# Kernel tuning notes

Measured on AMD Instinct MI355X. Metric: run time of the kernel, lower is better.

## Reference

```python
import jax, jax.numpy as jnp
import numpy as np

H = 1024        # hidden_size
F = 4096        # intermediate_size
E = 8           # num_local_experts
TOP_K = 2       # num_experts_per_tok
B, S = 1, 2048


def setup_inputs() -> dict:
    key = jax.random.key(0)
    k0, k1, k2, k3 = jax.random.split(key, 4)
    hidden_states = jax.random.normal(k0, (B, S, H), dtype=jnp.float32)
    # torch nn.Linear weights: gate [E_out, in]; experts stacked on leading axis
    gate_w = jax.random.normal(k1, (E, H), dtype=jnp.float32) * 0.02
    gate_up_w = jax.random.normal(k2, (E, 2 * F, H), dtype=jnp.float32) * 0.02
    down_w = jax.random.normal(k3, (E, H, F), dtype=jnp.float32) * 0.02
    return {"hidden_states": hidden_states, "gate_w": gate_w,
            "gate_up_w": gate_up_w, "down_w": down_w}


def reference(hidden_states, gate_w, gate_up_w, down_w):
    b, s, h = hidden_states.shape
    x = hidden_states.reshape(-1, h)                      # [T, H]
    # router: softmax in float32, top-k, renormalize
    router_logits = x @ gate_w.T                          # [T, E]
    probs = jax.nn.softmax(router_logits.astype(jnp.float32), axis=-1)
    topw, sel = jax.lax.top_k(probs, TOP_K)               # [T, K]
    topw = topw / jnp.sum(topw, axis=-1, keepdims=True)
    topw = topw.astype(x.dtype)
    # combine weights [T, E]: zero for unselected experts -> same math as
    # the per-expert gather/scatter loop (full capacity, no dropped tokens)
    combine = jnp.sum(jax.nn.one_hot(sel, E, dtype=x.dtype) * topw[..., None], axis=1)
    # all experts on all tokens (dense-equivalent of masked dispatch)
    gu = jnp.einsum('th,efh->etf', x, gate_up_w)          # [E, T, 2F]
    gate, up = gu[..., :F], gu[..., F:]
    hact = up * jax.nn.gelu(gate, approximate=False)      # [E, T, F]
    expert_out = jnp.einsum('etf,ehf->eth', hact, down_w) # [E, T, H]
    out = jnp.einsum('eth,te->th', expert_out, combine)   # [T, H]
    return out.reshape(b, s, h)
```

## Files before the change

kernel.cpp:

```cpp
#include <hip/hip_runtime.h>

#define Hdim 1024
#define Fdim 4096
#define NE   8
#define NT   2048
#define MT_MAX 16
#define KSPLIT 2

typedef __attribute__((ext_vector_type(8))) short short8;
typedef __attribute__((ext_vector_type(4))) short short4v;
typedef __attribute__((ext_vector_type(4))) float f32x4;

__device__ __forceinline__ unsigned short bf16r(float f) {
  union { float fv; unsigned u; } v; v.fv = f;
  unsigned u = v.u;
  return (unsigned short)((u + 0x7FFFu + ((u >> 16) & 1u)) >> 16);
}

__global__ void k_router(const float* __restrict__ x, const float* __restrict__ gw,
                         int* __restrict__ counts, int* __restrict__ sel,
                         float* __restrict__ selw) {
  int wave = threadIdx.x >> 6;
  int l    = threadIdx.x & 63;
  int t    = blockIdx.x * 4 + wave;
  const float* xp = x + (size_t)t * Hdim;
  float acc[NE];
#pragma unroll
  for (int e = 0; e < NE; e++) acc[e] = 0.f;
  for (int h = l; h < Hdim; h += 64) {
    float xv = xp[h];
#pragma unroll
    for (int e = 0; e < NE; e++) acc[e] += xv * gw[e * Hdim + h];
  }
#pragma unroll
  for (int e = 0; e < NE; e++) {
    float v = acc[e];
#pragma unroll
    for (int off = 32; off > 0; off >>= 1) v += __shfl_down(v, off, 64);
    acc[e] = v;
  }
  if (l == 0) {
    int b0 = 0; float v0 = acc[0];
    for (int e = 1; e < NE; e++) if (acc[e] > v0) { v0 = acc[e]; b0 = e; }
    int b1 = -1; float v1 = -1e30f;
    for (int e = 0; e < NE; e++) if (e != b0 && acc[e] > v1) { v1 = acc[e]; b1 = e; }
    float w0 = 1.f / (1.f + expf(v1 - v0));
    atomicAdd(&counts[b0], 1);
    atomicAdd(&counts[b1], 1);
    sel[2 * t]     = b0;
    sel[2 * t + 1] = b1;
    selw[2 * t]     = w0;
    selw[2 * t + 1] = 1.f - w0;
  }
}

__global__ void k_scatter(const int* __restrict__ counts, const int* __restrict__ sel,
                          const float* __restrict__ selw, int* __restrict__ offsets,
                          int* __restrict__ rowids, float* __restrict__ pairw,
                          int* __restrict__ tok2slot) {
  __shared__ int soff[NE];
  __shared__ int scur[NE];
  if (threadIdx.x == 0) {
    int s = 0;
    for (int e = 0; e < NE; e++) { soff[e] = s; offsets[e] = s; s += counts[e]; scur[e] = 0; }
  }
  __syncthreads();
  for (int t = threadIdx.x; t < NT; t += blockDim.x) {
#pragma unroll
    for (int j = 0; j < 2; j++) {
      int e = sel[2 * t + j];
      int p = atomicAdd(&scur[e], 1);
      int slot = soff[e] + p;
      rowids[slot]        = t;
      pairw[slot]         = selw[2 * t + j];
      tok2slot[2 * t + j] = slot;
    }
  }
}

__global__ __launch_bounds__(256, 2)
void k_gate_up(const float* __restrict__ x, const float* __restrict__ gup,
               const int* __restrict__ counts, const int* __restrict__ offsets,
               const int* __restrict__ rowids, unsigned short* __restrict__ hact) {
  int e  = blockIdx.y >> 4;
  int mt = blockIdx.y & 15;
  int n  = counts[e];
  if (mt * 128 >= n) return;
  int base = offsets[e];
  int row0 = mt * 128;
  int f0   = blockIdx.x * 64;

  __shared__ __align__(16) unsigned short As[128][40];
  __shared__ __align__(16) unsigned short Bs[128][40];
  __shared__ int rid[128];

  int tid = threadIdx.x;
  if (tid < 128) {
    int r = row0 + tid;
    rid[tid] = (r < n) ? rowids[base + r] : rowids[base];
  }
  __syncthreads();

  int kc   = (tid & 7) * 4;
  int trow = tid >> 3;
  const float* ap[4];
  const float* bp[4];
#pragma unroll
  for (int p = 0; p < 4; p++) {
    int ar = p * 32 + trow;
    ap[p] = x + (size_t)rid[ar] * Hdim + kc;
    int f = (ar < 64) ? (f0 + ar) : (Fdim + f0 + (ar - 64));
    bp[p] = gup + ((size_t)e * 2 * Fdim + f) * Hdim + kc;
  }

  int wave = tid >> 6, lane = tid & 63;
  int wy = wave >> 1, wx = wave & 1;
  int lrow = lane & 15, lk = (lane >> 4) * 8;
  f32x4 acc[4][4] = {};

  float4 ra[4], rb[4];
#pragma unroll
  for (int p = 0; p < 4; p++) { ra[p] = *(const float4*)(ap[p]); rb[p] = *(const float4*)(bp[p]); }

  for (int k0 = 0; k0 < Hdim; k0 += 32) {
    __syncthreads();
#pragma unroll
    for (int p = 0; p < 4; p++) {
      int ar = p * 32 + trow;
      short4v sa;
      sa.x = (short)bf16r(ra[p].x); sa.y = (short)bf16r(ra[p].y);
      sa.z = (short)bf16r(ra[p].z); sa.w = (short)bf16r(ra[p].w);
      *(short4v*)&As[ar][kc] = sa;
      short4v sb;
      sb.x = (short)bf16r(rb[p].x); sb.y = (short)bf16r(rb[p].y);
      sb.z = (short)bf16r(rb[p].z); sb.w = (short)bf16r(rb[p].w);
      *(short4v*)&Bs[ar][kc] = sb;
    }
    if (k0 + 32 < Hdim) {
#pragma unroll
      for (int p = 0; p < 4; p++) {
        ra[p] = *(const float4*)(ap[p] + k0 + 32);
        rb[p] = *(const float4*)(bp[p] + k0 + 32);
      }
    }
    __syncthreads();
    short8 a[4], b[4];
#pragma unroll
    for (int i = 0; i < 4; i++) a[i] = *(const short8*)&As[wy * 64 + i * 16 + lrow][lk];
    b[0] = *(const short8*)&Bs[wx * 32 + lrow][lk];
    b[1] = *(const short8*)&Bs[wx * 32 + 16 + lrow][lk];
    b[2] = *(const short8*)&Bs[64 + wx * 32 + lrow][lk];
    b[3] = *(const short8*)&Bs[64 + wx * 32 + 16 + lrow][lk];
#pragma unroll
    for (int i = 0; i < 4; i++)
#pragma unroll
      for (int j = 0; j < 4; j++)
        acc[i][j] = __builtin_amdgcn_mfma_f32_16x16x32_bf16(a[i], b[j], acc[i][j], 0, 0, 0);
  }

  int quad = lane >> 4;
#pragma unroll
  for (int i = 0; i < 4; i++) {
#pragma unroll
    for (int r = 0; r < 4; r++) {
      int rl = row0 + wy * 64 + i * 16 + quad * 4 + r;
      if (rl < n) {
        size_t rowoff = (size_t)(base + rl) * Fdim + f0 + wx * 32;
#pragma unroll
        for (int j = 0; j < 2; j++) {
          float g = acc[i][j][r];
          float u = acc[i][j + 2][r];
          float ge = 0.5f * g * (1.f + erff(g * 0.70710678118654752f));
          hact[rowoff + j * 16 + lrow] = bf16r(u * ge);
        }
      }
    }
  }
}

__global__ __launch_bounds__(256, 2)
void k_down(const unsigned short* __restrict__ hact, const float* __restrict__ dw,
            const int* __restrict__ counts, const int* __restrict__ offsets,
            const int* __restrict__ rowids, const float* __restrict__ pairw,
            float* __restrict__ part) {
  int e  = blockIdx.y >> 4;
  int mt = blockIdx.y & 15;
  int n  = counts[e];
  if (mt * 128 >= n) return;
  int base = offsets[e];
  int row0 = mt * 128;
  int h0   = blockIdx.x * 128;
  const int KC = Fdim / KSPLIT;
  int kbeg = blockIdx.z * KC;
  int kend = kbeg + KC;

  __shared__ __align__(16) unsigned short As[128][72];
  __shared__ __align__(16) unsigned short Bs[128][72];

  int tid = threadIdx.x;
  int wave = tid >> 6, lane = tid & 63;
  int wy = wave >> 1, wx = wave & 1;
  int lrow = lane & 15, lkq = (lane >> 4) * 8;

  const unsigned short* asrc[4];
#pragma unroll
  for (int p = 0; p < 4; p++) {
    int idx = p * 256 + tid;
    int row = idx >> 3, seg = idx & 7;
    int slot = base + row0 + row;
    if (slot > NT * 2 - 1) slot = NT * 2 - 1;
    asrc[p] = hact + (size_t)slot * Fdim + seg * 8;
  }
  const float* bsrc[8];
#pragma unroll
  for (int p = 0; p < 8; p++) {
    int idx = p * 256 + tid;
    int row = idx >> 4, seg = idx & 15;
    bsrc[p] = dw + ((size_t)e * Hdim + h0 + row) * Fdim + seg * 4;
  }

  int4   raw[4];
  float4 rbw[8];
#pragma unroll
  for (int p = 0; p < 4; p++) raw[p] = *(const int4*)(asrc[p] + kbeg);
#pragma unroll
  for (int p = 0; p < 8; p++) rbw[p] = *(const float4*)(bsrc[p] + kbeg);

  f32x4 acc[4][4] = {};
  for (int k0 = kbeg; k0 < kend; k0 += 64) {
    __syncthreads();
#pragma unroll
    for (int p = 0; p < 4; p++) {
      int idx = p * 256 + tid;
      int row = idx >> 3, seg = idx & 7;
      *(int4*)&As[row][seg * 8] = raw[p];
    }
#pragma unroll
    for (int p = 0; p < 8; p++) {
      int idx = p * 256 + tid;
      int row = idx >> 4, seg = idx & 15;
      short4v sb;
      sb.x = (short)bf16r(rbw[p].x); sb.y = (short)bf16r(rbw[p].y);
      sb.z = (short)bf16r(rbw[p].z); sb.w = (short)bf16r(rbw[p].w);
      *(short4v*)&Bs[row][seg * 4] = sb;
    }
    if (k0 + 64 < kend) {
#pragma unroll
      for (int p = 0; p < 4; p++) raw[p] = *(const int4*)(asrc[p] + k0 + 64);
#pragma unroll
      for (int p = 0; p < 8; p++) rbw[p] = *(const float4*)(bsrc[p] + k0 + 64);
    }
    __syncthreads();
#pragma unroll
    for (int ks = 0; ks < 2; ks++) {
      short8 a[4], b[4];
#pragma unroll
      for (int i = 0; i < 4; i++) a[i] = *(const short8*)&As[wy * 64 + i * 16 + lrow][ks * 32 + lkq];
#pragma unroll
      for (int j = 0; j < 4; j++) b[j] = *(const short8*)&Bs[wx * 64 + j * 16 + lrow][ks * 32 + lkq];
#pragma unroll
      for (int i = 0; i < 4; i++)
#pragma unroll
        for (int j = 0; j < 4; j++)
          acc[i][j] = __builtin_amdgcn_mfma_f32_16x16x32_bf16(a[i], b[j], acc[i][j], 0, 0, 0);
    }
  }

  int quad = lane >> 4;
#pragma unroll
  for (int i = 0; i < 4; i++) {
#pragma unroll
    for (int r = 0; r < 4; r++) {
      int rl = row0 + wy * 64 + i * 16 + quad * 4 + r;
      if (rl < n) {
        int slot = base + rl;
        float wv = pairw[slot];
        float* op = part + ((size_t)blockIdx.z * (NT * 2) + slot) * Hdim + h0 + wx * 64;
#pragma unroll
        for (int j = 0; j < 4; j++)
          op[j * 16 + lrow] = wv * acc[i][j][r];
      }
    }
  }
}

__global__ __launch_bounds__(256)
void k_combine(const float* __restrict__ part, const int* __restrict__ tok2slot,
               float* __restrict__ out) {
  int idx = blockIdx.x * 256 + threadIdx.x;
  int t  = idx >> 8;
  int hc = (idx & 255) << 2;
  int s0 = tok2slot[2 * t];
  int s1 = tok2slot[2 * t + 1];
  float4 a = *(const float4*)&part[(size_t)s0 * Hdim + hc];
  float4 b = *(const float4*)&part[((size_t)(NT * 2) + s0) * Hdim + hc];
  float4 c = *(const float4*)&part[(size_t)s1 * Hdim + hc];
  float4 d = *(const float4*)&part[((size_t)(NT * 2) + s1) * Hdim + hc];
  float4 s;
  s.x = (a.x + b.x) + (c.x + d.x);
  s.y = (a.y + b.y) + (c.y + d.y);
  s.z = (a.z + b.z) + (c.z + d.z);
  s.w = (a.w + b.w) + (c.w + d.w);
  *(float4*)&out[(size_t)t * Hdim + hc] = s;
}

extern "C" void kernel_launch(void* const* d_in, const int* in_sizes, int n_in,
                              void* d_out, int out_size, void* d_ws, size_t ws_size,
                              hipStream_t stream) {
  const float* x   = (const float*)d_in[0];
  const float* gw  = (const float*)d_in[1];
  const float* gup = (const float*)d_in[2];
  const float* dwn = (const float*)d_in[3];
  float* out = (float*)d_out;

  char* ws = (char*)d_ws;
  int*   counts   = (int*)(ws + 0);
  int*   offsets  = (int*)(ws + 128);
  int*   sel      = (int*)(ws + 4096);
  float* selw     = (float*)(ws + 4096 + 16384);
  int*   rowids   = (int*)(ws + 4096 + 32768);
  float* pairw    = (float*)(ws + 4096 + 49152);
  int*   tok2slot = (int*)(ws + 4096 + 65536);
  unsigned short* hact = (unsigned short*)(ws + (1 << 20));
  float* part = (float*)(ws + (1 << 20) + ((size_t)32 << 20));

  hipMemsetAsync(ws, 0, 4096, stream);

  k_router<<<NT / 4, 256, 0, stream>>>(x, gw, counts, sel, selw);
  k_scatter<<<1, 1024, 0, stream>>>(counts, sel, selw, offsets, rowids, pairw, tok2slot);
  k_gate_up<<<dim3(Fdim / 64, NE * MT_MAX), 256, 0, stream>>>(x, gup, counts, offsets, rowids, hact);
  k_down<<<dim3(Hdim / 128, NE * MT_MAX, KSPLIT), 256, 0, stream>>>(hact, dwn, counts, offsets, rowids, pairw, part);
  k_combine<<<NT * Hdim / 4 / 256, 256, 0, stream>>>(part, tok2slot, out);
}
```

Measured before the change: 761.4 us.

## Pre-convert activations and weights to bf16 and load tiles via global_load_lds

Adds a conversion kernel that casts x, gate_up and down weights to bf16 in workspace before each GEMM. The GEMMs then stream bf16 tiles directly into LDS with global_load_lds, using an XOR swizzle instead of padding to avoid bank conflicts, and drop the per-tile in-register conversion. Inside the GEMMs this halves the bytes read per weight tile and removes the conversion ALU work. In exchange there are extra full passes that read the fp32 weights and write bf16 copies on every call, the load loop is no longer register-prefetched, and the fast path runs only when the workspace is large enough.

```diff
diff --git a/kernel.cpp b/kernel.cpp
--- a/kernel.cpp
+++ b/kernel.cpp
@@ -15,6 +15,24 @@
   union { float fv; unsigned u; } v; v.fv = f;
   unsigned u = v.u;
   return (unsigned short)((u + 0x7FFFu + ((u >> 16) & 1u)) >> 16);
+}
+
+__device__ __forceinline__ void gl_lds16(const void* g, void* l) {
+  __builtin_amdgcn_global_load_lds(
+      (const __attribute__((address_space(1))) unsigned int*)g,
+      (__attribute__((address_space(3))) unsigned int*)l, 16, 0, 0);
+}
+
+__global__ __launch_bounds__(256)
+void k_cvt(const float* __restrict__ src, unsigned short* __restrict__ dst, int n4) {
+  int stride = gridDim.x * 256;
+  for (int i = blockIdx.x * 256 + threadIdx.x; i < n4; i += stride) {
+    float4 v = *(const float4*)(src + (size_t)i * 4);
+    short4v s;
+    s.x = (short)bf16r(v.x); s.y = (short)bf16r(v.y);
+    s.z = (short)bf16r(v.z); s.w = (short)bf16r(v.w);
+    *(short4v*)(dst + (size_t)i * 4) = s;
+  }
 }
 
 __global__ void k_router(const float* __restrict__ x, const float* __restrict__ gw,
@@ -79,9 +97,9 @@
 }
 
 __global__ __launch_bounds__(256, 2)
-void k_gate_up(const float* __restrict__ x, const float* __restrict__ gup,
-               const int* __restrict__ counts, const int* __restrict__ offsets,
-               const int* __restrict__ rowids, unsigned short* __restrict__ hact) {
+void k_gate_up_bf(const unsigned short* __restrict__ xbf, const unsigned short* __restrict__ wbf,
+                  const int* __restrict__ counts, const int* __restrict__ offsets,
+                  const int* __restrict__ rowids, unsigned short* __restrict__ hact) {
   int e  = blockIdx.y >> 4;
   int mt = blockIdx.y & 15;
   int n  = counts[e];
@@ -90,8 +108,8 @@
   int row0 = mt * 128;
   int f0   = blockIdx.x * 64;
 
-  __shared__ __align__(16) unsigned short As[128][40];
-  __shared__ __align__(16) unsigned short Bs[128][40];
+  __shared__ __align__(16) unsigned short As[128][64];
+  __shared__ __align__(16) unsigned short Bs[128][64];
   __shared__ int rid[128];
 
   int tid = threadIdx.x;
@@ -101,61 +119,54 @@
   }
   __syncthreads();
 
-  int kc   = (tid & 7) * 4;
-  int trow = tid >> 3;
-  const float* ap[4];
-  const float* bp[4];
+  int crow  = tid >> 3;
+  int cphys = tid & 7;
+  const unsigned short* sa[4];
+  const unsigned short* sb[4];
 #pragma unroll
   for (int p = 0; p < 4; p++) {
-    int ar = p * 32 + trow;
-    ap[p] = x + (size_t)rid[ar] * Hdim + kc;
-    int f = (ar < 64) ? (f0 + ar) : (Fdim + f0 + (ar - 64));
-    bp[p] = gup + ((size_t)e * 2 * Fdim + f) * Hdim + kc;
-  }
-
-  int wave = tid >> 6, lane = tid & 63;
-  int wy = wave >> 1, wx = wave & 1;
-  int lrow = lane & 15, lk = (lane >> 4) * 8;
+    int R = p * 32 + crow;
+    int csrc = cphys ^ (R & 7);
+    sa[p] = xbf + (size_t)rid[R] * Hdim + csrc * 8;
+    int fr = (R < 64) ? (f0 + R) : (Fdim + f0 + (R - 64));
+    sb[p] = wbf + ((size_t)e * 2 * Fdim + fr) * Hdim + csrc * 8;
+  }
+  int w = tid >> 6, lane = tid & 63;
+  unsigned short* da[4];
+  unsigned short* db[4];
+#pragma unroll
+  for (int p = 0; p < 4; p++) {
+    da[p] = &As[0][0] + p * 2048 + w * 512;
+    db[p] = &Bs[0][0] + p * 2048 + w * 512;
+  }
+
+  int wy = w >> 1, wx = w & 1;
+  int lrow = lane & 15, cq = lane >> 4;
   f32x4 acc[4][4] = {};
 
-  float4 ra[4], rb[4];
-#pragma unroll
-  for (int p = 0; p < 4; p++) { ra[p] = *(const float4*)(ap[p]); rb[p] = *(const float4*)(bp[p]); }
-
-  for (int k0 = 0; k0 < Hdim; k0 += 32) {
-    __syncthreads();
-#pragma unroll
-    for (int p = 0; p < 4; p++) {
-      int ar = p * 32 + trow;
-      short4v sa;
-      sa.x = (short)bf16r(ra[p].x); sa.y = (short)bf16r(ra[p].y);
-      sa.z = (short)bf16r(ra[p].z); sa.w = (short)bf16r(ra[p].w);
-      *(short4v*)&As[ar][kc] = sa;
-      short4v sb;
-      sb.x = (short)bf16r(rb[p].x); sb.y = (short)bf16r(rb[p].y);
-      sb.z = (short)bf16r(rb[p].z); sb.w = (short)bf16r(rb[p].w);
-      *(short4v*)&Bs[ar][kc] = sb;
-    }
-    if (k0 + 32 < Hdim) {
-#pragma unroll
-      for (int p = 0; p < 4; p++) {
-        ra[p] = *(const float4*)(ap[p] + k0 + 32);
-        rb[p] = *(const float4*)(bp[p] + k0 + 32);
-      }
-    }
-    __syncthreads();
-    short8 a[4], b[4];
-#pragma unroll
-    for (int i = 0; i < 4; i++) a[i] = *(const short8*)&As[wy * 64 + i * 16 + lrow][lk];
-    b[0] = *(const short8*)&Bs[wx * 32 + lrow][lk];
-    b[1] = *(const short8*)&Bs[wx * 32 + 16 + lrow][lk];
-    b[2] = *(const short8*)&Bs[64 + wx * 32 + lrow][lk];
-    b[3] = *(const short8*)&Bs[64 + wx * 32 + 16 + lrow][lk];
-#pragma unroll
-    for (int i = 0; i < 4; i++)
-#pragma unroll
-      for (int j = 0; j < 4; j++)
-        acc[i][j] = __builtin_amdgcn_mfma_f32_16x16x32_bf16(a[i], b[j], acc[i][j], 0, 0, 0);
+  for (int k0 = 0; k0 < Hdim; k0 += 64) {
+#pragma unroll
+    for (int p = 0; p < 4; p++) gl_lds16(sa[p] + k0, da[p]);
+#pragma unroll
+    for (int p = 0; p < 4; p++) gl_lds16(sb[p] + k0, db[p]);
+    __syncthreads();
+#pragma unroll
+    for (int ks = 0; ks < 2; ks++) {
+      int soff = ((ks * 4 + cq) ^ (lrow & 7)) * 8;
+      short8 a[4], b[4];
+#pragma unroll
+      for (int i = 0; i < 4; i++) a[i] = *(const short8*)&As[wy * 64 + i * 16 + lrow][soff];
+      b[0] = *(const short8*)&Bs[wx * 32 + lrow][soff];
+      b[1] = *(const short8*)&Bs[wx * 32 + 16 + lrow][soff];
+      b[2] = *(const short8*)&Bs[64 + wx * 32 + lrow][soff];
+      b[3] = *(const short8*)&Bs[64 + wx * 32 + 16 + lrow][soff];
+#pragma unroll
+      for (int i = 0; i < 4; i++)
+#pragma unroll
+        for (int j = 0; j < 4; j++)
+          acc[i][j] = __builtin_amdgcn_mfma_f32_16x16x32_bf16(a[i], b[j], acc[i][j], 0, 0, 0);
+    }
+    __syncthreads();
   }
 
   int quad = lane >> 4;
@@ -179,10 +190,9 @@
 }
 
 __global__ __launch_bounds__(256, 2)
-void k_down(const unsigned short* __restrict__ hact, const float* __restrict__ dw,
-            const int* __restrict__ counts, const int* __restrict__ offsets,
-            const int* __restrict__ rowids, const float* __restrict__ pairw,
-            float* __restrict__ part) {
+void k_down_bf(const unsigned short* __restrict__ hact, const unsigned short* __restrict__ dbf,
+               const int* __restrict__ counts, const int* __restrict__ offsets,
+               const float* __restrict__ pairw, float* __restrict__ part) {
   int e  = blockIdx.y >> 4;
   int mt = blockIdx.y & 15;
   int n  = counts[e];
@@ -194,6 +204,192 @@
   int kbeg = blockIdx.z * KC;
   int kend = kbeg + KC;
 
+  __shared__ __align__(16) unsigned short As[128][64];
+  __shared__ __align__(16) unsigned short Bs[128][64];
+
+  int tid = threadIdx.x;
+  int crow  = tid >> 3;
+  int cphys = tid & 7;
+  const unsigned short* sa[4];
+  const unsigned short* sb[4];
+#pragma unroll
+  for (int p = 0; p < 4; p++) {
+    int R = p * 32 + crow;
+    int csrc = cphys ^ (R & 7);
+    int slot = base + row0 + R;
+    if (slot > NT * 2 - 1) slot = NT * 2 - 1;
+    sa[p] = hact + (size_t)slot * Fdim + csrc * 8;
+    sb[p] = dbf + ((size_t)e * Hdim + h0 + R) * Fdim + csrc * 8;
+  }
+  int w = tid >> 6, lane = tid & 63;
+  unsigned short* da[4];
+  unsigned short* db[4];
+#pragma unroll
+  for (int p = 0; p < 4; p++) {
+    da[p] = &As[0][0] + p * 2048 + w * 512;
+    db[p] = &Bs[0][0] + p * 2048 + w * 512;
+  }
+
+  int wy = w >> 1, wx = w & 1;
+  int lrow = lane & 15, cq = lane >> 4;
+  f32x4 acc[4][4] = {};
+
+  for (int k0 = kbeg; k0 < kend; k0 += 64) {
+#pragma unroll
+    for (int p = 0; p < 4; p++) gl_lds16(sa[p] + k0, da[p]);
+#pragma unroll
+    for (int p = 0; p < 4; p++) gl_lds16(sb[p] + k0, db[p]);
+    __syncthreads();
+#pragma unroll
+    for (int ks = 0; ks < 2; ks++) {
+      int soff = ((ks * 4 + cq) ^ (lrow & 7)) * 8;
+      short8 a[4], b[4];
+#pragma unroll
+      for (int i = 0; i < 4; i++) a[i] = *(const short8*)&As[wy * 64 + i * 16 + lrow][soff];
+#pragma unroll
+      for (int j = 0; j < 4; j++) b[j] = *(const short8*)&Bs[wx * 64 + j * 16 + lrow][soff];
+#pragma unroll
+      for (int i = 0; i < 4; i++)
+#pragma unroll
+        for (int j = 0; j < 4; j++)
+          acc[i][j] = __builtin_amdgcn_mfma_f32_16x16x32_bf16(a[i], b[j], acc[i][j], 0, 0, 0);
+    }
+    __syncthreads();
+  }
+
+  int quad = lane >> 4;
+#pragma unroll
+  for (int i = 0; i < 4; i++) {
+#pragma unroll
+    for (int r = 0; r < 4; r++) {
+      int rl = row0 + wy * 64 + i * 16 + quad * 4 + r;
+      if (rl < n) {
+        int slot = base + rl;
+        float wv = pairw[slot];
+        float* op = part + ((size_t)blockIdx.z * (NT * 2) + slot) * Hdim + h0 + wx * 64;
+#pragma unroll
+        for (int j = 0; j < 4; j++)
+          op[j * 16 + lrow] = wv * acc[i][j][r];
+      }
+    }
+  }
+}
+
+__global__ __launch_bounds__(256, 2)
+void k_gate_up_v1(const float* __restrict__ x, const float* __restrict__ gup,
+                  const int* __restrict__ counts, const int* __restrict__ offsets,
+                  const int* __restrict__ rowids, unsigned short* __restrict__ hact) {
+  int e  = blockIdx.y >> 4;
+  int mt = blockIdx.y & 15;
+  int n  = counts[e];
+  if (mt * 128 >= n) return;
+  int base = offsets[e];
+  int row0 = mt * 128;
+  int f0   = blockIdx.x * 64;
+
+  __shared__ __align__(16) unsigned short As[128][40];
+  __shared__ __align__(16) unsigned short Bs[128][40];
+  __shared__ int rid[128];
+
+  int tid = threadIdx.x;
+  if (tid < 128) {
+    int r = row0 + tid;
+    rid[tid] = (r < n) ? rowids[base + r] : rowids[base];
+  }
+  __syncthreads();
+
+  int kc   = (tid & 7) * 4;
+  int trow = tid >> 3;
+  const float* ap[4];
+  const float* bp[4];
+#pragma unroll
+  for (int p = 0; p < 4; p++) {
+    int ar = p * 32 + trow;
+    ap[p] = x + (size_t)rid[ar] * Hdim + kc;
+    int f = (ar < 64) ? (f0 + ar) : (Fdim + f0 + (ar - 64));
+    bp[p] = gup + ((size_t)e * 2 * Fdim + f) * Hdim + kc;
+  }
+
+  int wave = tid >> 6, lane = tid & 63;
+  int wy = wave >> 1, wx = wave & 1;
+  int lrow = lane & 15, lk = (lane >> 4) * 8;
+  f32x4 acc[4][4] = {};
+
+  float4 ra[4], rb[4];
+#pragma unroll
+  for (int p = 0; p < 4; p++) { ra[p] = *(const float4*)(ap[p]); rb[p] = *(const float4*)(bp[p]); }
+
+  for (int k0 = 0; k0 < Hdim; k0 += 32) {
+    __syncthreads();
+#pragma unroll
+    for (int p = 0; p < 4; p++) {
+      int ar = p * 32 + trow;
+      short4v sa;
+      sa.x = (short)bf16r(ra[p].x); sa.y = (short)bf16r(ra[p].y);
+      sa.z = (short)bf16r(ra[p].z); sa.w = (short)bf16r(ra[p].w);
+      *(short4v*)&As[ar][kc] = sa;
+      short4v sbv;
+      sbv.x = (short)bf16r(rb[p].x); sbv.y = (short)bf16r(rb[p].y);
+      sbv.z = (short)bf16r(rb[p].z); sbv.w = (short)bf16r(rb[p].w);
+      *(short4v*)&Bs[ar][kc] = sbv;
+    }
+    if (k0 + 32 < Hdim) {
+#pragma unroll
+      for (int p = 0; p < 4; p++) {
+        ra[p] = *(const float4*)(ap[p] + k0 + 32);
+        rb[p] = *(const float4*)(bp[p] + k0 + 32);
+      }
+    }
+    __syncthreads();
+    short8 a[4], b[4];
+#pragma unroll
+    for (int i = 0; i < 4; i++) a[i] = *(const short8*)&As[wy * 64 + i * 16 + lrow][lk];
+    b[0] = *(const short8*)&Bs[wx * 32 + lrow][lk];
+    b[1] = *(const short8*)&Bs[wx * 32 + 16 + lrow][lk];
+    b[2] = *(const short8*)&Bs[64 + wx * 32 + lrow][lk];
+    b[3] = *(const short8*)&Bs[64 + wx * 32 + 16 + lrow][lk];
+#pragma unroll
+    for (int i = 0; i < 4; i++)
+#pragma unroll
+      for (int j = 0; j < 4; j++)
+        acc[i][j] = __builtin_amdgcn_mfma_f32_16x16x32_bf16(a[i], b[j], acc[i][j], 0, 0, 0);
+  }
+
+  int quad = lane >> 4;
+#pragma unroll
+  for (int i = 0; i < 4; i++) {
+#pragma unroll
+    for (int r = 0; r < 4; r++) {
+      int rl = row0 + wy * 64 + i * 16 + quad * 4 + r;
+      if (rl < n) {
+        size_t rowoff = (size_t)(base + rl) * Fdim + f0 + wx * 32;
+#pragma unroll
+        for (int j = 0; j < 2; j++) {
+          float g = acc[i][j][r];
+          float u = acc[i][j + 2][r];
+          float ge = 0.5f * g * (1.f + erff(g * 0.70710678118654752f));
+          hact[rowoff + j * 16 + lrow] = bf16r(u * ge);
+        }
+      }
+    }
+  }
+}
+
+__global__ __launch_bounds__(256, 2)
+void k_down_v1(const unsigned short* __restrict__ hact, const float* __restrict__ dw,
+               const int* __restrict__ counts, const int* __restrict__ offsets,
+               const float* __restrict__ pairw, float* __restrict__ part) {
+  int e  = blockIdx.y >> 4;
+  int mt = blockIdx.y & 15;
+  int n  = counts[e];
+  if (mt * 128 >= n) return;
+  int base = offsets[e];
+  int row0 = mt * 128;
+  int h0   = blockIdx.x * 128;
+  const int KC = Fdim / KSPLIT;
+  int kbeg = blockIdx.z * KC;
+  int kend = kbeg + KC;
+
   __shared__ __align__(16) unsigned short As[128][72];
   __shared__ __align__(16) unsigned short Bs[128][72];
 
@@ -239,10 +435,10 @@
     for (int p = 0; p < 8; p++) {
       int idx = p * 256 + tid;
       int row = idx >> 4, seg = idx & 15;
-      short4v sb;
-      sb.x = (short)bf16r(rbw[p].x); sb.y = (short)bf16r(rbw[p].y);
-      sb.z = (short)bf16r(rbw[p].z); sb.w = (short)bf16r(rbw[p].w);
-      *(short4v*)&Bs[row][seg * 4] = sb;
+      short4v sbv;
+      sbv.x = (short)bf16r(rbw[p].x); sbv.y = (short)bf16r(rbw[p].y);
+      sbv.z = (short)bf16r(rbw[p].z); sbv.w = (short)bf16r(rbw[p].w);
+      *(short4v*)&Bs[row][seg * 4] = sbv;
     }
     if (k0 + 64 < kend) {
 #pragma unroll
@@ -323,12 +519,26 @@
   int*   tok2slot = (int*)(ws + 4096 + 65536);
   unsigned short* hact = (unsigned short*)(ws + (1 << 20));
   float* part = (float*)(ws + (1 << 20) + ((size_t)32 << 20));
+  unsigned short* xbf = (unsigned short*)(ws + (1 << 20) + ((size_t)64 << 20));
+  unsigned short* wbf = (unsigned short*)(ws + (1 << 20) + ((size_t)68 << 20));
+  unsigned short* dbf = wbf;
+
+  const size_t NEED = (size_t)(1 << 20) + ((size_t)68 << 20) + ((size_t)128 << 20);
 
   hipMemsetAsync(ws, 0, 4096, stream);
 
   k_router<<<NT / 4, 256, 0, stream>>>(x, gw, counts, sel, selw);
   k_scatter<<<1, 1024, 0, stream>>>(counts, sel, selw, offsets, rowids, pairw, tok2slot);
-  k_gate_up<<<dim3(Fdim / 64, NE * MT_MAX), 256, 0, stream>>>(x, gup, counts, offsets, rowids, hact);
-  k_down<<<dim3(Hdim / 128, NE * MT_MAX, KSPLIT), 256, 0, stream>>>(hact, dwn, counts, offsets, rowids, pairw, part);
+
+  if (ws_size >= NEED) {
+    k_cvt<<<2048, 256, 0, stream>>>(x, xbf, NT * Hdim / 4);
+    k_cvt<<<2048, 256, 0, stream>>>(gup, wbf, NE * 2 * Fdim * Hdim / 4);
+    k_gate_up_bf<<<dim3(Fdim / 64, NE * MT_MAX), 256, 0, stream>>>(xbf, wbf, counts, offsets, rowids, hact);
+    k_cvt<<<2048, 256, 0, stream>>>(dwn, dbf, NE * Hdim * Fdim / 4);
+    k_down_bf<<<dim3(Hdim / 128, NE * MT_MAX, KSPLIT), 256, 0, stream>>>(hact, dbf, counts, offsets, pairw, part);
+  } else {
+    k_gate_up_v1<<<dim3(Fdim / 64, NE * MT_MAX), 256, 0, stream>>>(x, gup, counts, offsets, rowids, hact);
+    k_down_v1<<<dim3(Hdim / 128, NE * MT_MAX, KSPLIT), 256, 0, stream>>>(hact, dwn, counts, offsets, pairw, part);
+  }
   k_combine<<<NT * Hdim / 4 / 256, 256, 0, stream>>>(part, tok2slot, out);
 }
```

Result: faster. 709.8 us (-6.8%).
